# Optimization experiments

Measured on AMD Instinct MI355X. Metric: run time of the kernel, lower is better.

Reference implementation:

```python
import jax, jax.numpy as jnp
import numpy as np

N_ATOMS = 64
N_SAMPLES = 2 ** 15
SAMPLERATE = 22050
N_RES = 4096
N_ROOMS = 8
N_COEFFS = N_SAMPLES // 2 + 1


def make_waves():
    # musical_scale_hz(21, 106, 4096//4) -> 4 waveform families (sine, saw, square, triangle)
    n_steps = N_RES // 4
    midi = np.linspace(21.0, 106.0, n_steps)
    f0 = 440.0 * 2.0 ** ((midi - 69.0) / 12.0)
    rps = ((f0 / (SAMPLERATE / 2.0)) * np.pi).astype(np.float32)
    rad = rps[:, None] * np.arange(N_SAMPLES, dtype=np.float32)[None, :]
    sine = np.sin(rad)
    t = rad / (2.0 * np.pi)
    saw = (2.0 * (t - np.floor(t + 0.5))).astype(np.float32)
    sq = np.sign(sine).astype(np.float32)
    tri = (2.0 * np.abs(saw) - 1.0).astype(np.float32)
    return jnp.asarray(np.concatenate([sine, saw, sq, tri], 0).reshape(1, N_RES, N_SAMPLES))


def pdf2(means, stds, n):
    # gaussian pdf evaluated on linspace(0,1,n); means/stds: (1, A)
    rng = jnp.linspace(0.0, 1.0, n)
    mu = means[..., None]
    sd = stds[..., None]
    return jnp.exp(-0.5 * ((rng - mu) / sd) ** 2) / (sd * jnp.sqrt(2.0 * jnp.pi))


def linear_interp(x, n_out):
    # F.interpolate(mode='linear', align_corners=False) on last axis; x: (b, a, f)
    f = x.shape[-1]
    pos = (jnp.arange(n_out) + 0.5) * (f / n_out) - 0.5
    pos = jnp.clip(pos, 0.0, f - 1)
    i0 = jnp.floor(pos).astype(jnp.int32)
    i1 = jnp.minimum(i0 + 1, f - 1)
    w = (pos - i0).astype(x.dtype)
    return x[..., i0] * (1.0 - w) + x[..., i1] * w


def exponential_decay(decay_values, n_atoms, n_frames, base_resonance, n_samples):
    dv = jax.nn.sigmoid(decay_values.reshape(-1, n_atoms, 1))
    dv = jnp.broadcast_to(dv, (dv.shape[0], n_atoms, n_frames))
    decay = base_resonance + dv * (1.0 - base_resonance) * 0.95
    decay = jnp.exp(jnp.cumsum(jnp.log(decay + 1e-12), axis=-1))
    return linear_interp(decay, n_samples)


def fft_convolve(a, b):
    # zero-pad to 2N, multiply spectra, take first N samples
    n = a.shape[-1]
    pa = jnp.pad(a, ((0, 0), (0, 0), (0, n)))
    pb = jnp.pad(b, ((0, 0), (0, 0), (0, n)))
    spec = jnp.fft.rfft(pa, axis=-1) * jnp.fft.rfft(pb, axis=-1)
    return jnp.fft.irfft(spec, n=2 * n, axis=-1)[..., :n]


def layer_norm(x, w, b, eps=1e-5):
    m = jnp.mean(x, axis=-1, keepdims=True)
    v = jnp.var(x, axis=-1, keepdims=True)
    return (x - m) / jnp.sqrt(v + eps) * w + b


def sparse_softmax_st(x):
    soft = jax.nn.softmax(x, axis=-1)
    hard = jax.nn.one_hot(jnp.argmax(x, axis=-1), x.shape[-1], dtype=x.dtype)
    return hard + soft - jax.lax.stop_gradient(soft)


def model_forward(x, mix, decays, filter_decays, resonance_choice, noise_filter,
                  resonance_filter, resonance_filter2, env, amplitudes, verb_params,
                  noise, waves, ln_w, ln_b, mix_w1, mix_w2, room_w1, room_w2, room_irs):
    overall_mix = jax.nn.softmax(mix, axis=-1)                                   # (1,A,2)
    resonances = jnp.einsum('bar,brn->ban', jax.nn.relu(resonance_choice), waves)  # (1,A,N)

    # band-pass filtered noise (gaussian filter in frequency domain)
    noise_spec = jnp.fft.rfft(noise, axis=-1)
    noise_filt = pdf2(noise_filter[:, :, 0], jnp.abs(noise_filter[:, :, 1]) + 1e-12, N_COEFFS)
    filtered_noise = jnp.fft.irfft(noise_spec * noise_filt, n=N_SAMPLES, axis=-1)

    res_spec = jnp.fft.rfft(resonances, axis=-1)
    rf1 = pdf2(jnp.zeros_like(resonance_filter[:, :, 0]),
               jnp.abs(resonance_filter[:, :, 1]) + 1e-12, N_COEFFS)
    filtered_resonance = jnp.fft.irfft(res_spec * rf1, n=N_SAMPLES, axis=-1)
    rf2 = pdf2(jnp.zeros_like(resonance_filter2[:, :, 0]),
               jnp.abs(resonance_filter2[:, :, 1]) + 1e-12, N_COEFFS)
    filt_res_2 = jnp.fft.irfft(res_spec * rf2, n=N_SAMPLES, axis=-1)

    filt_crossfade = exponential_decay(filter_decays, N_ATOMS, 128, 0.02, N_SAMPLES)
    decay_env = exponential_decay(decays, N_ATOMS, 128, 0.02, N_SAMPLES)
    decaying_resonance = filtered_resonance * decay_env
    decaying_resonance2 = filt_res_2 * decay_env

    # gaussian envelope branch (gaussian_envelope = True)
    envelopes = pdf2(env[:, :, 0], jnp.abs(env[:, :, 1] + 1e-12) * 0.1, N_SAMPLES)
    positioned_noise = filtered_noise * envelopes

    res = fft_convolve(positioned_noise, decaying_resonance)
    res2 = fft_convolve(positioned_noise, decaying_resonance2)
    mixed = filt_crossfade * res + (1.0 - filt_crossfade) * res2

    final = positioned_noise * overall_mix[:, :, 0:1] + mixed * overall_mix[:, :, 1:2]
    final = final / (jnp.linalg.norm(final, axis=-1, keepdims=True) + 1e-8)
    amps = jnp.abs(amplitudes)
    final = final * amps

    # ReverbGenerator: layernorm -> small MLPs -> hard room choice -> fft convolve with IR
    h = layer_norm(verb_params, ln_w, ln_b)
    mix_v = jax.nn.sigmoid(jax.nn.leaky_relu(h @ mix_w1) @ mix_w2)               # (1,A,1)
    room_logits = jax.nn.leaky_relu(h @ room_w1) @ room_w2                        # (1,A,R)
    room = sparse_softmax_st(room_logits)
    ir = jnp.einsum('bar,rn->ban', room, room_irs)
    wet = fft_convolve(final, ir)
    out = final * mix_v + wet * (1.0 - mix_v)
    return out, amps


def setup_inputs() -> dict:
    key = jax.random.key(0)
    ks = jax.random.split(key, 20)
    return {
        'x': jax.random.normal(ks[0], (1, 1), jnp.float32),
        'mix': jax.random.uniform(ks[1], (1, N_ATOMS, 2), jnp.float32),
        'decays': jax.random.uniform(ks[2], (1, N_ATOMS, 1), jnp.float32, -6.0, 6.0),
        'filter_decays': jax.random.uniform(ks[3], (1, N_ATOMS, 1), jnp.float32, -6.0, 6.0),
        'resonance_choice': jax.random.uniform(ks[4], (1, N_ATOMS, N_RES), jnp.float32),
        'noise_filter': jax.random.uniform(ks[5], (1, N_ATOMS, 2), jnp.float32),
        'resonance_filter': jax.random.uniform(ks[6], (1, N_ATOMS, 2), jnp.float32),
        'resonance_filter2': jax.random.uniform(ks[7], (1, N_ATOMS, 2), jnp.float32),
        'env': jax.random.uniform(ks[8], (1, N_ATOMS, 2), jnp.float32),
        'amplitudes': jax.random.uniform(ks[9], (1, N_ATOMS, 1), jnp.float32) ** 2,
        'verb_params': jax.random.uniform(ks[10], (1, N_ATOMS, 4), jnp.float32, -1.0, 1.0),
        'noise': jax.random.uniform(ks[11], (1, N_ATOMS, N_SAMPLES), jnp.float32, -1.0, 1.0),
        'waves': make_waves(),
        'ln_w': jnp.ones((4,), jnp.float32),
        'ln_b': jnp.zeros((4,), jnp.float32),
        'mix_w1': jax.random.normal(ks[12], (4, 4), jnp.float32) * 0.1,
        'mix_w2': jax.random.normal(ks[13], (4, 1), jnp.float32) * 0.1,
        'room_w1': jax.random.normal(ks[14], (4, 4), jnp.float32) * 0.1,
        'room_w2': jax.random.normal(ks[15], (4, N_ROOMS), jnp.float32) * 0.1,
        'room_irs': jax.random.normal(ks[16], (N_ROOMS, N_SAMPLES), jnp.float32) * 0.01,
    }


def reference(x, mix, decays, filter_decays, resonance_choice, noise_filter,
              resonance_filter, resonance_filter2, env, amplitudes, verb_params,
              noise, waves, ln_w, ln_b, mix_w1, mix_w2, room_w1, room_w2, room_irs):
    return model_forward(x, mix, decays, filter_decays, resonance_choice, noise_filter,
                         resonance_filter, resonance_filter2, env, amplitudes, verb_params,
                         noise, waves, ln_w, ln_b, mix_w1, mix_w2, room_w1, room_w2, room_irs)
```

## Files before the change

### kernel.cpp

```cpp
#include <hip/hip_runtime.h>


typedef __attribute__((ext_vector_type(8))) short bf16x8;
typedef __attribute__((ext_vector_type(4))) float f32x4;

constexpr int SC_OM0   = 0;
constexpr int SC_OM1   = 64;
constexpr int SC_NFMU  = 128;
constexpr int SC_NFSD  = 192;
constexpr int SC_RF1SD = 256;
constexpr int SC_RF2SD = 320;
constexpr int SC_ENVMU = 384;
constexpr int SC_ENVSD = 448;
constexpr int SC_AMPS  = 512;
constexpr int SC_MIXV  = 576;
constexpr int SC_ROOM  = 832;
constexpr int SC_PSS   = 1024;
constexpr int SC_DTAB  = 4096;
constexpr int SC_FTAB  = 12288;
constexpr int SC_RPS   = 20480;

constexpr size_t OFF_SCAL = 0;
constexpr size_t OFF_CT   = 65536;
constexpr size_t OFF_P    = 327680;
constexpr size_t OFF_DS   = 8716288;
constexpr size_t OFF_RP   = OFF_DS;
constexpr size_t OFF_W64  = 17104896;
constexpr size_t OFF_NSS  = OFF_W64;
constexpr size_t OFF_W2   = OFF_W64 + 4194304;
constexpr size_t OFF_RSS  = 25493504;
constexpr size_t OFF_FINU = OFF_RSS;
constexpr size_t OFF_W1   = 29687808;
constexpr size_t OFF_FN   = 38076416;
constexpr size_t OFF_FRP  = 40173568;
constexpr size_t OFF_IRS  = 44367872;
constexpr size_t WS_FLOATS= 45416448;

__device__ __forceinline__ float2 cmul(float2 a, float2 b) {
  return make_float2(a.x*b.x - a.y*b.y, a.x*b.y + a.y*b.x);
}

__device__ __forceinline__ short f2bf(float x) {
  unsigned u = __float_as_uint(x);
  u = (u + 0x7FFFu + ((u >> 16) & 1u)) >> 16;
  return (short)u;
}
__device__ __forceinline__ float bf2f(short s) {
  return __uint_as_float((unsigned)(unsigned short)s << 16);
}
__device__ __forceinline__ unsigned pk2(float2 v) {
  return (unsigned)(unsigned short)f2bf(v.x)
       | ((unsigned)(unsigned short)f2bf(v.y) << 16);
}
__device__ __forceinline__ float2 upk2(unsigned u) {
  return make_float2(__uint_as_float(u << 16),
                     __uint_as_float(u & 0xFFFF0000u));
}

__device__ __forceinline__ void dft16(float2 d[16], float ei)
{
  const float CA[4] = {1.0f, 0.92387953251128674f, 0.70710678118654752f, 0.38268343236508977f};
  const float SA[4] = {0.0f, 0.38268343236508977f, 0.70710678118654752f, 0.92387953251128674f};
  const float CB[4] = {1.0f, 0.70710678118654752f, 0.0f, -0.70710678118654752f};
  const float SB[4] = {0.0f, 0.70710678118654752f, 1.0f, 0.70710678118654752f};
  float2 e[16];
  #pragma unroll
  for (int q = 0; q < 4; ++q) {
    float2 x0 = d[q], x1 = d[q+4], x2 = d[q+8], x3 = d[q+12];
    float ca = CA[q], sa = ei*SA[q], cb = CB[q], sb = ei*SB[q];
    float2 sum1 = make_float2(x0.x+x2.x, x0.y+x2.y);
    float2 d1   = make_float2(x0.x-x2.x, x0.y-x2.y);
    float2 dif1 = make_float2(d1.x*ca - d1.y*sa, d1.x*sa + d1.y*ca);
    float2 sum2 = make_float2(x1.x+x3.x, x1.y+x3.y);
    float2 d2   = make_float2(x1.x-x3.x, x1.y-x3.y);
    float2 dt   = make_float2(d2.x*ca - d2.y*sa, d2.x*sa + d2.y*ca);
    float2 dif2 = make_float2(-ei*dt.y, ei*dt.x);
    float2 Dm   = make_float2(sum1.x-sum2.x, sum1.y-sum2.y);
    float2 Dm2  = make_float2(dif1.x-dif2.x, dif1.y-dif2.y);
    e[4*q+0] = make_float2(sum1.x+sum2.x, sum1.y+sum2.y);
    e[4*q+1] = make_float2(dif1.x+dif2.x, dif1.y+dif2.y);
    e[4*q+2] = make_float2(Dm.x*cb - Dm.y*sb, Dm.x*sb + Dm.y*cb);
    e[4*q+3] = make_float2(Dm2.x*cb - Dm2.y*sb, Dm2.x*sb + Dm2.y*cb);
  }
  #pragma unroll
  for (int q = 0; q < 4; ++q) {
    float2 x0 = e[q], x1 = e[q+4], x2 = e[q+8], x3 = e[q+12];
    float2 sum1 = make_float2(x0.x+x2.x, x0.y+x2.y);
    float2 dif1 = make_float2(x0.x-x2.x, x0.y-x2.y);
    float2 sum2 = make_float2(x1.x+x3.x, x1.y+x3.y);
    float2 d2   = make_float2(x1.x-x3.x, x1.y-x3.y);
    float2 dif2 = make_float2(-ei*d2.y, ei*d2.x);
    d[q]    = make_float2(sum1.x+sum2.x, sum1.y+sum2.y);
    d[q+4]  = make_float2(dif1.x+dif2.x, dif1.y+dif2.y);
    d[q+8]  = make_float2(sum1.x-sum2.x, sum1.y-sum2.y);
    d[q+12] = make_float2(dif1.x-dif2.x, dif1.y-dif2.y);
  }
}

__device__ __forceinline__ void twiddleB(float2 d[16], int u, float dir2pi)
{
  float sn1, cs1;
  __sincosf(dir2pi * ((float)u * (1.0f/256.0f)), &sn1, &cs1);
  float2 w1 = make_float2(cs1, sn1);
  float2 tw = w1;
  #pragma unroll
  for (int k = 1; k < 16; ++k) { d[k] = cmul(d[k], tw); tw = cmul(tw, w1); }
}

template<int LEN>
__device__ float2* lds_fft(float2* src, float2* dst,
                           const float2* __restrict__ T256,
                           float dsign, float ei)
{
  constexpr int QB  = LEN >> 2;
  constexpr int FPT = (16 * QB) >> 8;
  constexpr int NST = (LEN == 256) ? 4 : 3;
  int n = LEN, s = 1, ls = 0;
  int sh = (LEN == 256) ? 0 : 1;

  if (LEN == 128) {
    constexpr int HB = LEN >> 1;
    constexpr int BPT = (16 * HB) >> 8;
    __syncthreads();
    #pragma unroll
    for (int b = 0; b < BPT; ++b) {
      int g = threadIdx.x + (b << 8);
      int row = g / HB;
      int beta = g & (HB - 1);
      float2 tj = T256[beta << 1];
      float cs = tj.x, sn = dsign * tj.y;
      float2 av = src[row*LEN + (beta ^ row)];
      float2 bv = src[row*LEN + ((beta + HB) ^ row)];
      float2 sum = make_float2(av.x + bv.x, av.y + bv.y);
      float2 dif = make_float2(av.x - bv.x, av.y - bv.y);
      float2 tw  = make_float2(dif.x*cs - dif.y*sn, dif.x*sn + dif.y*cs);
      dst[row*LEN + ((2*beta)     ^ row)] = sum;
      dst[row*LEN + ((2*beta + 1) ^ row)] = tw;
    }
    float2* t = src; src = dst; dst = t;
    n = 64; s = 2; ls = 1; sh = 2;
  }

  for (int st = 0; st < NST; ++st) {
    __syncthreads();
    #pragma unroll
    for (int b = 0; b < FPT; ++b) {
      int g   = threadIdx.x + (b << 8);
      int row = g / QB;
      int q   = g & (QB - 1);
      int p1  = q >> ls;
      int blo = q & (s - 1);
      int base = row * LEN;
      float2 x0 = src[base + ( q         ^ row)];
      float2 x1 = src[base + ((q +   QB) ^ row)];
      float2 x2 = src[base + ((q + 2*QB) ^ row)];
      float2 x3 = src[base + ((q + 3*QB) ^ row)];
      float2 tA = T256[p1 << sh];
      float caA = tA.x, saA = dsign * tA.y;
      float2 tB = T256[p1 << (sh + 1)];
      float caB = tB.x, saB = dsign * tB.y;
      float2 sum1 = make_float2(x0.x + x2.x, x0.y + x2.y);
      float2 d1   = make_float2(x0.x - x2.x, x0.y - x2.y);
      float2 dif1 = make_float2(d1.x*caA - d1.y*saA, d1.x*saA + d1.y*caA);
      float2 sum2 = make_float2(x1.x + x3.x, x1.y + x3.y);
      float2 d2   = make_float2(x1.x - x3.x, x1.y - x3.y);
      float2 dt   = make_float2(d2.x*caA - d2.y*saA, d2.x*saA + d2.y*caA);
      float2 dif2 = make_float2(-ei * dt.y, ei * dt.x);
      float2 S  = make_float2(sum1.x + sum2.x, sum1.y + sum2.y);
      float2 Dm = make_float2(sum1.x - sum2.x, sum1.y - sum2.y);
      float2 D  = make_float2(Dm.x*caB - Dm.y*saB, Dm.x*saB + Dm.y*caB);
      float2 S2 = make_float2(dif1.x + dif2.x, dif1.y + dif2.y);
      float2 Dm2= make_float2(dif1.x - dif2.x, dif1.y - dif2.y);
      float2 D2 = make_float2(Dm2.x*caB - Dm2.y*saB, Dm2.x*saB + Dm2.y*caB);
      int w0 = (p1 << (ls + 2)) | blo;
      dst[base + ( w0          ^ row)] = S;
      dst[base + ((w0 +     s) ^ row)] = S2;
      dst[base + ((w0 + 2 * s) ^ row)] = D;
      dst[base + ((w0 + 3 * s) ^ row)] = D2;
    }
    float2* t = src; src = dst; dst = t;
    n >>= 2; s <<= 2; ls += 2; sh += 2;
  }
  __syncthreads();
  return src;
}

__global__ __launch_bounds__(256) void k_fft_s256_DsPI(
    unsigned* __restrict__ Ds, unsigned* __restrict__ P,
    unsigned* __restrict__ IRS,
    const unsigned* __restrict__ FRP, const short* __restrict__ fnb,
    const float* __restrict__ rirs, const float* __restrict__ scal)
{
  constexpr int N = 65536, NH = 32768;
  constexpr float FWD = -6.283185307179586f;
  __shared__ float2 X[16*16*17];
  __shared__ float2 T256[256];
  __shared__ float2 TN[256];
  const int mode = (blockIdx.y < 64) ? 0 : ((blockIdx.y < 128) ? 1 : 2);
  const int a = (mode == 0) ? blockIdx.y : ((mode == 1) ? blockIdx.y - 64 : blockIdx.y - 128);
  const int n1base = blockIdx.x << 4;
  const int r = threadIdx.x & 15;
  const int u = threadIdx.x >> 4;

  {
    float ang = FWD * ((float)threadIdx.x * (1.0f/256.0f));
    float sn, cs; __sincosf(ang, &sn, &cs);
    T256[threadIdx.x] = make_float2(cs, sn);
    float ang2 = FWD * ((float)threadIdx.x * (1.0f/(float)N));
    float sn2, cs2; __sincosf(ang2, &sn2, &cs2);
    TN[threadIdx.x] = make_float2(cs2, sn2);
  }

  float emu = 0.f, esd = 1.f, egp = 0.f;
  if (mode == 1) {
    emu = scal[SC_ENVMU + a];
    esd = scal[SC_ENVSD + a];
    egp = 0.3989422804014327f / esd;
  }

  float2 d[16];
  #pragma unroll
  for (int m = 0; m < 16; ++m) {
    int j = u + (m << 4);
    int n = n1base + r + 256 * j;
    float2 v = make_float2(0.0f, 0.0f);
    if (n < NH) {
      if (mode == 0) {
        float pos = ((float)n + 0.5f) * (1.0f/256.0f) - 0.5f;
        pos = fminf(fmaxf(pos, 0.0f), 127.0f);
        int i0 = (int)pos;
        float w = pos - (float)i0;
        int i1 = (i0 + 1 < 127) ? i0 + 1 : 127;
        const float* dt = scal + SC_DTAB + a*128;
        float de = dt[i0]*(1.0f-w) + dt[i1]*w;
        float2 fr = upk2(FRP[(size_t)a * NH + n]);
        v = make_float2(fr.x * de, fr.y * de);
      } else if (mode == 1) {
        float uu = (float)n * (1.0f / 32767.0f);
        float te = (uu - emu) / esd;
        float envv = __expf(-0.5f * te * te) * egp;
        v = make_float2(bf2f(fnb[(size_t)a * NH + n]) * envv, 0.0f);
      } else {
        v = make_float2(rirs[(size_t)a * NH + n], 0.0f);
      }
    }
    d[m] = v;
  }

  dft16(d, -1.0f);
  twiddleB(d, u, FWD);
  #pragma unroll
  for (int k = 0; k < 16; ++k) X[(u*16 + k)*17 + r] = d[k];
  __syncthreads();
  #pragma unroll
  for (int m = 0; m < 16; ++m) d[m] = X[(m*16 + u)*17 + r];
  dft16(d, -1.0f);

  unsigned* outp = (mode == 0) ? Ds : ((mode == 1) ? P : IRS);
  #pragma unroll
  for (int k1 = 0; k1 < 16; ++k1) {
    int j = u + (k1 << 4);
    int n = n1base + r + 256 * j;
    int aa = (n1base + r) * j;
    float2 tw = cmul(T256[(aa >> 8) & 255], TN[aa & 255]);
    outp[(size_t)a * N + n] = pk2(cmul(d[k1], tw));
  }
}

__global__ __launch_bounds__(256) void k_fft_s128_first(
    unsigned* __restrict__ RSs, unsigned* __restrict__ NSs,
    const short* __restrict__ rez, const float* __restrict__ noise)
{
  constexpr int N1 = 128, N = 32768;
  constexpr float FWD = -6.283185307179586f;
  __shared__ float2 X[16*16*17];
  __shared__ float2 T256[256];
  __shared__ float2 TN[128];
  const bool isRS = blockIdx.y < 64;
  const int a = isRS ? blockIdx.y : blockIdx.y - 64;
  const int n1base = blockIdx.x << 4;
  const int r = threadIdx.x & 15;
  const int u = threadIdx.x >> 4;

  {
    float ang = FWD * ((float)threadIdx.x * (1.0f/256.0f));
    float sn, cs; __sincosf(ang, &sn, &cs);
    T256[threadIdx.x] = make_float2(cs, sn);
    if (threadIdx.x < 128) {
      float ang2 = FWD * ((float)threadIdx.x * (1.0f/(float)N));
      float sn2, cs2; __sincosf(ang2, &sn2, &cs2);
      TN[threadIdx.x] = make_float2(cs2, sn2);
    }
  }

  float2 d[16];
  #pragma unroll
  for (int m = 0; m < 16; ++m) {
    int j = u + (m << 4);
    int n = n1base + r + N1 * j;
    float x = isRS ? (bf2f(rez[(size_t)a * N + n]) +
                      bf2f(rez[(size_t)(64 + a) * N + n]))
                   : noise[(size_t)a * N + n];
    d[m] = make_float2(x, 0.0f);
  }

  dft16(d, -1.0f);
  twiddleB(d, u, FWD);
  #pragma unroll
  for (int k = 0; k < 16; ++k) X[(u*16 + k)*17 + r] = d[k];
  __syncthreads();
  #pragma unroll
  for (int m = 0; m < 16; ++m) d[m] = X[(m*16 + u)*17 + r];
  dft16(d, -1.0f);

  unsigned* outp = isRS ? RSs : NSs;
  #pragma unroll
  for (int k1 = 0; k1 < 16; ++k1) {
    int j = u + (k1 << 4);
    int n = n1base + r + N1 * j;
    int aa = (n1base + r) * j;
    float2 tw = cmul(T256[(aa >> 7) & 255], TN[aa & 127]);
    outp[(size_t)a * N + n] = pk2(cmul(d[k1], tw));
  }
}

__global__ __launch_bounds__(256) void k_fft_m128_both(
    const unsigned* __restrict__ RSs, const unsigned* __restrict__ NSs,
    unsigned* __restrict__ W1, unsigned* __restrict__ W2,
    const float* __restrict__ scal)
{
  constexpr int N1 = 128;
  constexpr int N = N1 * 256;
  constexpr int ITERS = (16 * N1) >> 8;
  constexpr int LOG2N1 = 7;
  constexpr float FWD = -6.283185307179586f;
  constexpr float IVD = +6.283185307179586f;
  __shared__ float2 A[16 * N1];
  __shared__ float2 B[16 * N1];
  __shared__ float2 T256[256];
  __shared__ float2 TN[N1];
  const bool isRS = blockIdx.y < 64;
  const int a = isRS ? blockIdx.y : blockIdx.y - 64;
  const int colbase = blockIdx.x << 4;

  {
    float ang = FWD * ((float)threadIdx.x * (1.0f/256.0f));
    float sn, cs; __sincosf(ang, &sn, &cs);
    T256[threadIdx.x] = make_float2(cs, sn);
    if (threadIdx.x < N1) {
      float ang2 = IVD * ((float)threadIdx.x * (1.0f/(float)N));
      float sn2, cs2; __sincosf(ang2, &sn2, &cs2);
      TN[threadIdx.x] = make_float2(cs2, sn2);
    }
  }

  float mu = 0.f, isd1 = 0.f, g1 = 0.f, isd2 = 0.f, g2 = 0.f;
  if (isRS) {
    float s1 = scal[SC_RF1SD + a], s2 = scal[SC_RF2SD + a];
    isd1 = 1.0f/s1; g1 = 0.3989422804014327f/s1;
    isd2 = 1.0f/s2; g2 = 0.3989422804014327f/s2;
  } else {
    float sd = scal[SC_NFSD + a]; mu = scal[SC_NFMU + a];
    isd1 = 1.0f/sd; g1 = 0.3989422804014327f/sd;
  }
  const unsigned* zin = (isRS ? RSs : NSs) + (size_t)a * N;
  unsigned* out = (isRS ? W1 : W2) + (size_t)a * N;

  #pragma unroll
  for (int it = 0; it < ITERS; ++it) {
    int flat = threadIdx.x + (it << 8);
    int c = flat / N1, j = flat & (N1 - 1);
    A[c*N1 + (j ^ c)] = upk2(zin[(size_t)(colbase + c) * N1 + j]);
  }
  float2* cur = lds_fft<N1>(A, B, T256, 1.0f, -1.0f);
  float2* alt = (cur == A) ? B : A;

  #pragma unroll
  for (int it = 0; it < ITERS; ++it) {
    int flat = threadIdx.x + (it << 8);
    int c = flat / N1, j = flat & (N1 - 1);
    int idx = c*N1 + (j ^ c);
    float2 v = cur[idx];
    int k  = (colbase + c) + (j << 8);
    int kk = (k <= N - k) ? k : N - k;
    if (isRS) {
      float fr = (float)kk * (2.0f/(float)N);
      float t1 = fr * isd1, t2 = fr * isd2;
      float ga = __expf(-0.5f * t1 * t1) * g1;
      float gb = __expf(-0.5f * t2 * t2) * g2;
      v = make_float2(v.x*ga - v.y*gb, v.x*gb + v.y*ga);
    } else {
      float t = ((float)kk * (2.0f/(float)N) - mu) * isd1;
      float g = __expf(-0.5f * t * t) * g1;
      v.x *= g; v.y *= g;
    }
    cur[idx] = v;
  }

  float2* r2 = lds_fft<N1>(cur, alt, T256, -1.0f, 1.0f);

  #pragma unroll
  for (int it = 0; it < ITERS; ++it) {
    int flat = threadIdx.x + (it << 8);
    int c = flat / N1, j = flat & (N1 - 1);
    float2 v = r2[c*N1 + (j ^ c)];
    int aa = j * (colbase + c);
    float2 t1 = T256[(aa >> LOG2N1) & 255];
    t1.y = -t1.y;
    float2 tw = cmul(t1, TN[aa & (N1 - 1)]);
    out[(size_t)(colbase + c) * N1 + j] = pk2(cmul(v, tw));
  }
}

__global__ __launch_bounds__(256) void k_fft_s128_last(
    const unsigned* __restrict__ W1, const unsigned* __restrict__ W2,
    unsigned* __restrict__ FRP, short* __restrict__ fnb)
{
  constexpr int N1 = 128, N = 32768;
  constexpr float IVD = +6.283185307179586f;
  constexpr float S32 = 1.0f / 32768.0f;
  __shared__ float2 X[16*16*17];
  const bool isRS = blockIdx.y < 64;
  const int a = isRS ? blockIdx.y : blockIdx.y - 64;
  const int n1base = blockIdx.x << 4;
  const int r = threadIdx.x & 15;
  const int u = threadIdx.x >> 4;

  const unsigned* cb = (isRS ? W1 : W2) + (size_t)a * N;
  float2 d[16];
  #pragma unroll
  for (int m = 0; m < 16; ++m) {
    int j = u + (m << 4);
    d[m] = upk2(cb[n1base + r + N1 * j]);
  }
  dft16(d, 1.0f);
  twiddleB(d, u, IVD);
  #pragma unroll
  for (int k = 0; k < 16; ++k) X[(u*16 + k)*17 + r] = d[k];
  __syncthreads();
  #pragma unroll
  for (int m = 0; m < 16; ++m) d[m] = X[(m*16 + u)*17 + r];
  dft16(d, 1.0f);

  #pragma unroll
  for (int k1 = 0; k1 < 16; ++k1) {
    int j = u + (k1 << 4);
    int n = n1base + r + N1 * j;
    if (isRS) {
      FRP[(size_t)a * N + n] = pk2(make_float2(d[k1].x * S32, d[k1].y * S32));
    } else {
      fnb[(size_t)a * N + n] = f2bf(d[k1].x * S32);
    }
  }
}

__global__ __launch_bounds__(256) void k_fft_mid256dual(
    const unsigned* __restrict__ zin, const unsigned* __restrict__ zin2half,
    unsigned* __restrict__ out1, const int* __restrict__ roomArr)
{
  constexpr int N = 65536;
  constexpr float FWD = -6.283185307179586f;
  constexpr float IVD = +6.283185307179586f;
  __shared__ float2 X[16*16*17];
  __shared__ float2 T256[256];
  __shared__ float2 TN[256];
  const int a = blockIdx.y;
  const int colbase = blockIdx.x << 4;
  const int u  = threadIdx.x & 15;
  const int rc = threadIdx.x >> 4;

  {
    float ang = FWD * ((float)threadIdx.x * (1.0f/256.0f));
    float sn, cs; __sincosf(ang, &sn, &cs);
    T256[threadIdx.x] = make_float2(cs, sn);
    float ang2 = IVD * ((float)threadIdx.x * (1.0f/(float)N));
    float sn2, cs2; __sincosf(ang2, &sn2, &cs2);
    TN[threadIdx.x] = make_float2(cs2, sn2);
  }
  __syncthreads();

  const unsigned* z2 = zin2half + (size_t)(roomArr ? roomArr[a] : a) * N;
  const size_t rowG = (size_t)a * N + (size_t)(colbase + rc) * 256;
  const size_t rowZ2 = (size_t)(colbase + rc) * 256;

  float2 d[16];
  #pragma unroll
  for (int m = 0; m < 16; ++m) d[m] = upk2(zin[rowG + u + (m << 4)]);
  dft16(d, -1.0f);
  twiddleB(d, u, FWD);
  #pragma unroll
  for (int k = 0; k < 16; ++k) X[(rc*16 + k)*17 + u] = d[k];
  #pragma unroll
  for (int m = 0; m < 16; ++m) d[m] = X[(rc*16 + u)*17 + m];
  dft16(d, -1.0f);

  float2 stash[16];
  #pragma unroll
  for (int k = 0; k < 16; ++k) stash[k] = d[k];
  #pragma unroll
  for (int m = 0; m < 16; ++m) d[m] = upk2(z2[rowZ2 + u + (m << 4)]);
  dft16(d, -1.0f);
  twiddleB(d, u, FWD);
  #pragma unroll
  for (int k = 0; k < 16; ++k) X[(rc*16 + k)*17 + u] = d[k];
  #pragma unroll
  for (int m = 0; m < 16; ++m) d[m] = X[(rc*16 + u)*17 + m];
  dft16(d, -1.0f);
  #pragma unroll
  for (int k = 0; k < 16; ++k) d[k] = cmul(stash[k], d[k]);

  dft16(d, 1.0f);
  twiddleB(d, u, IVD);
  #pragma unroll
  for (int k = 0; k < 16; ++k) X[(rc*16 + k)*17 + u] = d[k];
  #pragma unroll
  for (int m = 0; m < 16; ++m) d[m] = X[(rc*16 + u)*17 + m];
  dft16(d, 1.0f);

  #pragma unroll
  for (int k1 = 0; k1 < 16; ++k1) {
    int j = u + (k1 << 4);
    int aa = j * (colbase + rc);
    float2 t1 = T256[(aa >> 8) & 255];
    t1.y = -t1.y;
    float2 tw = cmul(t1, TN[aa & 255]);
    out1[rowG + j] = pk2(cmul(d[k1], tw));
  }
}

__global__ __launch_bounds__(256) void k_fft_out6fwd(
    const unsigned* __restrict__ W64in, const short* __restrict__ fnb,
    float* __restrict__ finU, float* __restrict__ scal,
    unsigned* __restrict__ DsOut)
{
  constexpr int N = 65536, NH = 32768;
  constexpr float FWD = -6.283185307179586f;
  constexpr float IVD = +6.283185307179586f;
  constexpr float S64 = 1.0f / 65536.0f;
  __shared__ float2 X[16*16*17];
  __shared__ float2 T256[256];
  __shared__ float2 TN[256];
  __shared__ float red[256];
  const int a = blockIdx.y;
  const int n1base = blockIdx.x << 4;
  const int r = threadIdx.x & 15;
  const int u = threadIdx.x >> 4;

  {
    float ang = FWD * ((float)threadIdx.x * (1.0f/256.0f));
    float sn, cs; __sincosf(ang, &sn, &cs);
    T256[threadIdx.x] = make_float2(cs, sn);
    float ang2 = FWD * ((float)threadIdx.x * (1.0f/(float)N));
    float sn2, cs2; __sincosf(ang2, &sn2, &cs2);
    TN[threadIdx.x] = make_float2(cs2, sn2);
  }

  const float emu = scal[SC_ENVMU + a];
  const float esd = scal[SC_ENVSD + a];
  const float egp = 0.3989422804014327f / esd;
  const float om0 = scal[SC_OM0 + a], om1 = scal[SC_OM1 + a];
  const float* ft = scal + SC_FTAB + a*128;

  float2 d[16];
  #pragma unroll
  for (int m = 0; m < 16; ++m) {
    int j = u + (m << 4);
    d[m] = upk2(W64in[(size_t)a * N + n1base + r + 256 * j]);
  }
  dft16(d, 1.0f);
  twiddleB(d, u, IVD);
  #pragma unroll
  for (int k = 0; k < 16; ++k) X[(u*16 + k)*17 + r] = d[k];
  __syncthreads();
  #pragma unroll
  for (int m = 0; m < 16; ++m) d[m] = X[(m*16 + u)*17 + r];
  dft16(d, 1.0f);

  float fv[8];
  float ss = 0.0f;
  #pragma unroll
  for (int k1 = 0; k1 < 8; ++k1) {
    int n = n1base + r + 256 * (u + (k1 << 4));
    float resv  = d[k1].x * S64;
    float res2v = d[k1].y * S64;
    float uu = (float)n * (1.0f / 32767.0f);
    float te = (uu - emu) / esd;
    float envv = __expf(-0.5f * te * te) * egp;
    float pnv = bf2f(fnb[(size_t)a * NH + n]) * envv;
    float pos = ((float)n + 0.5f) * (1.0f/256.0f) - 0.5f;
    pos = fminf(fmaxf(pos, 0.0f), 127.0f);
    int i0 = (int)pos;
    float w = pos - (float)i0;
    int i1 = (i0 + 1 < 127) ? i0 + 1 : 127;
    float fc = ft[i0]*(1.0f-w) + ft[i1]*w;
    float f = pnv*om0 + (fc*resv + (1.0f-fc)*res2v)*om1;
    finU[(size_t)a * NH + n] = f;
    fv[k1] = f;
    ss += f * f;
  }
  red[threadIdx.x] = ss;
  __syncthreads();
  for (int s = 128; s > 0; s >>= 1) {
    if (threadIdx.x < s) red[threadIdx.x] += red[threadIdx.x + s];
    __syncthreads();
  }
  if (threadIdx.x == 0) scal[SC_PSS + a*16 + blockIdx.x] = red[0];

  #pragma unroll
  for (int m = 0; m < 16; ++m)
    d[m] = (m < 8) ? make_float2(fv[m], 0.0f) : make_float2(0.0f, 0.0f);
  dft16(d, -1.0f);
  twiddleB(d, u, FWD);
  #pragma unroll
  for (int k = 0; k < 16; ++k) X[(u*16 + k)*17 + r] = d[k];
  __syncthreads();
  #pragma unroll
  for (int m = 0; m < 16; ++m) d[m] = X[(m*16 + u)*17 + r];
  dft16(d, -1.0f);

  #pragma unroll
  for (int k1 = 0; k1 < 16; ++k1) {
    int j = u + (k1 << 4);
    int n = n1base + r + 256 * j;
    int aa = (n1base + r) * j;
    float2 tw = cmul(T256[(aa >> 8) & 255], TN[aa & 255]);
    DsOut[(size_t)a * N + n] = pk2(cmul(d[k1], tw));
  }
}

__global__ __launch_bounds__(256) void k_fft_s256_out3(
    const unsigned* __restrict__ W64in, const float* __restrict__ finU,
    const float* __restrict__ scal, float* __restrict__ out)
{
  constexpr int N = 65536, NH = 32768;
  constexpr float IVD = +6.283185307179586f;
  constexpr float S64 = 1.0f / 65536.0f;
  __shared__ float2 X[16*16*17];
  const int a = blockIdx.y;
  const int n1base = blockIdx.x << 4;
  const int r = threadIdx.x & 15;
  const int u = threadIdx.x >> 4;

  float ss = 0.0f;
  #pragma unroll
  for (int i = 0; i < 16; ++i) ss += scal[SC_PSS + a*16 + i];
  float fscale = scal[SC_AMPS + a] / (sqrtf(ss) + 1e-8f);
  float mixv = scal[SC_MIXV + a];
  float w1 = fscale * (1.0f - mixv);
  float w0 = fscale * mixv;

  float2 d[16];
  #pragma unroll
  for (int m = 0; m < 16; ++m) {
    int j = u + (m << 4);
    d[m] = upk2(W64in[(size_t)a * N + n1base + r + 256 * j]);
  }
  dft16(d, 1.0f);
  twiddleB(d, u, IVD);
  #pragma unroll
  for (int k = 0; k < 16; ++k) X[(u*16 + k)*17 + r] = d[k];
  __syncthreads();
  #pragma unroll
  for (int m = 0; m < 16; ++m) d[m] = X[(m*16 + u)*17 + r];
  dft16(d, 1.0f);

  #pragma unroll
  for (int k1 = 0; k1 < 8; ++k1) {
    int n = n1base + r + 256 * (u + (k1 << 4));
    out[(size_t)a * NH + n] =
        d[k1].x * S64 * w1 + finU[(size_t)a * NH + n] * w0;
  }
}

__global__ void k_packA(const float* __restrict__ rc, short* __restrict__ ctb,
    const float* __restrict__ mix, const float* __restrict__ decays,
    const float* __restrict__ fdec, const float* __restrict__ nf,
    const float* __restrict__ rf1, const float* __restrict__ rf2,
    const float* __restrict__ env, const float* __restrict__ amplitudes,
    const float* __restrict__ verb, const float* __restrict__ ln_w,
    const float* __restrict__ ln_b, const float* __restrict__ mw1,
    const float* __restrict__ mw2, const float* __restrict__ rw1,
    const float* __restrict__ rw2, float* __restrict__ scal,
    float* __restrict__ dout)
{
  int o = blockIdx.x * 256 + threadIdx.x;
  {
    int m = o >> 12, k = o & 4095;
    int s = k >> 2, f = k & 3;
    float v = fmaxf(rc[m*4096 + f*1024 + s], 0.0f);
    ctb[o] = f2bf(v);
  }
  if (blockIdx.x < 4) {
    int idx = blockIdx.x * 256 + threadIdx.x;
    double step = 85.0 / 1023.0;
    double midi = (double)idx * step + 21.0;
    if (idx == 1023) midi = 106.0;
    double f0 = 440.0 * exp2((midi - 69.0) * (1.0 / 12.0));
    scal[SC_RPS + idx] = (float)((f0 / 11025.0) * 3.141592653589793);
  }
  if (blockIdx.x != 0 || threadIdx.x >= 64) return;
  int a = threadIdx.x;
  float m0 = mix[a*2+0], m1 = mix[a*2+1];
  float mx = fmaxf(m0, m1);
  float e0 = expf(m0 - mx), e1 = expf(m1 - mx);
  float inv = 1.0f / (e0 + e1);
  scal[SC_OM0+a] = e0 * inv;
  scal[SC_OM1+a] = e1 * inv;
  scal[SC_NFMU+a] = nf[a*2+0];
  scal[SC_NFSD+a] = fabsf(nf[a*2+1]) + 1e-12f;
  scal[SC_RF1SD+a] = fabsf(rf1[a*2+1]) + 1e-12f;
  scal[SC_RF2SD+a] = fabsf(rf2[a*2+1]) + 1e-12f;
  scal[SC_ENVMU+a] = env[a*2+0];
  scal[SC_ENVSD+a] = fabsf(env[a*2+1] + 1e-12f) * 0.1f;
  float amp = fabsf(amplitudes[a]);
  scal[SC_AMPS+a] = amp;
  dout[2097152 + a] = amp;
  float d  = 0.02f + (1.0f/(1.0f+expf(-decays[a]))) * (0.98f * 0.95f);
  float fd = 0.02f + (1.0f/(1.0f+expf(-fdec[a])))   * (0.98f * 0.95f);
  float pd = 1.0f, pf = 1.0f;
  for (int f = 0; f < 128; ++f) {
    pd *= d; pf *= fd;
    scal[SC_DTAB + a*128 + f] = pd;
    scal[SC_FTAB + a*128 + f] = pf;
  }
  float x0 = verb[a*4+0], x1 = verb[a*4+1], x2 = verb[a*4+2], x3 = verb[a*4+3];
  float mean = (x0+x1+x2+x3) * 0.25f;
  float d0 = x0-mean, d1 = x1-mean, d2 = x2-mean, d3 = x3-mean;
  float var = (d0*d0 + d1*d1 + d2*d2 + d3*d3) * 0.25f;
  float rs = 1.0f / sqrtf(var + 1e-5f);
  float h[4] = { d0*rs*ln_w[0]+ln_b[0], d1*rs*ln_w[1]+ln_b[1],
                 d2*rs*ln_w[2]+ln_b[2], d3*rs*ln_w[3]+ln_b[3] };
  float t[4], u[4];
  for (int j = 0; j < 4; ++j) {
    float s1 = 0.f, s2 = 0.f;
    for (int i2 = 0; i2 < 4; ++i2) {
      s1 += h[i2] * mw1[i2*4 + j];
      s2 += h[i2] * rw1[i2*4 + j];
    }
    t[j] = (s1 > 0.f) ? s1 : 0.01f*s1;
    u[j] = (s2 > 0.f) ? s2 : 0.01f*s2;
  }
  float ml = 0.f;
  for (int j = 0; j < 4; ++j) ml += t[j] * mw2[j];
  scal[SC_MIXV+a] = 1.0f / (1.0f + expf(-ml));
  float best = -1e30f; int bi = 0;
  for (int rr = 0; rr < 8; ++rr) {
    float lg = 0.f;
    for (int j = 0; j < 4; ++j) lg += u[j] * rw2[j*8 + rr];
    if (lg > best) { best = lg; bi = rr; }
  }
  ((int*)scal)[SC_ROOM + a] = bi;
}

__global__ __launch_bounds__(512) void k_gemm_mfma(
    const float* __restrict__ scal, const short* __restrict__ ctb,
    short* __restrict__ rp)
{
  const int t = threadIdx.x;
  const int w = t >> 6, lane = t & 63;
  const int ml = lane & 15, q = lane >> 4;
  const int col = blockIdx.x * 128 + w * 16 + ml;
  const int part = blockIdx.y;

  const float colf = (float)col;
  const float TWO_PI_F = 6.28318530717958647692f;
  const double INV_2PI = 0.15915494309189533577;

  f32x4 acc[4] = {};
  const short* abase = ctb + (size_t)ml * 4096 + (size_t)part * 2048 + q * 8;
  const float* rtab = scal + SC_RPS + part * 512;

  #define WAVE4(rps, b, off) { \
    float rad = (rps) * colf; \
    double dt = (double)rad * INV_2PI; \
    double frd = dt - floor(dt); \
    float sine = __sinf((float)frd * TWO_PI_F); \
    float sq = (rad == 0.0f) ? 0.0f : ((frd < 0.5) ? 1.0f : -1.0f); \
    float tt = rad / TWO_PI_F; \
    float saw = 2.0f * (tt - floorf(tt + 0.5f)); \
    float tri = 2.0f * fabsf(saw) - 1.0f; \
    b[off+0] = f2bf(sine); b[off+1] = f2bf(saw); \
    b[off+2] = f2bf(sq);   b[off+3] = f2bf(tri); }

  for (int kbl = 0; kbl < 64; ++kbl) {
    int sl = kbl * 8 + 2 * q;
    float rps0 = rtab[sl], rps1 = rtab[sl + 1];
    bf16x8 b;
    WAVE4(rps0, b, 0);
    WAVE4(rps1, b, 4);
    const short* ap = abase + (size_t)kbl * 32;
    acc[0] = __builtin_amdgcn_mfma_f32_16x16x32_bf16(*(const bf16x8*)(ap),                   b, acc[0], 0,0,0);
    acc[1] = __builtin_amdgcn_mfma_f32_16x16x32_bf16(*(const bf16x8*)(ap + (size_t)16*4096), b, acc[1], 0,0,0);
    acc[2] = __builtin_amdgcn_mfma_f32_16x16x32_bf16(*(const bf16x8*)(ap + (size_t)32*4096), b, acc[2], 0,0,0);
    acc[3] = __builtin_amdgcn_mfma_f32_16x16x32_bf16(*(const bf16x8*)(ap + (size_t)48*4096), b, acc[3], 0,0,0);
  }
  #undef WAVE4

  #pragma unroll
  for (int mt = 0; mt < 4; ++mt) {
    #pragma unroll
    for (int rr = 0; rr < 4; ++rr) {
      rp[(size_t)(part*64 + mt*16 + q*4 + rr) * 32768 + col] = f2bf(acc[mt][rr]);
    }
  }
}

extern "C" void kernel_launch(void* const* d_in, const int* in_sizes, int n_in,
                              void* d_out, int out_size, void* d_ws, size_t ws_size,
                              hipStream_t stream)
{
  const float* mix   = (const float*)d_in[1];
  const float* dec   = (const float*)d_in[2];
  const float* fdec  = (const float*)d_in[3];
  const float* rc    = (const float*)d_in[4];
  const float* nf    = (const float*)d_in[5];
  const float* rf1   = (const float*)d_in[6];
  const float* rf2   = (const float*)d_in[7];
  const float* env   = (const float*)d_in[8];
  const float* amps  = (const float*)d_in[9];
  const float* verb  = (const float*)d_in[10];
  const float* noise = (const float*)d_in[11];
  const float* lnw   = (const float*)d_in[13];
  const float* lnb   = (const float*)d_in[14];
  const float* mw1   = (const float*)d_in[15];
  const float* mw2   = (const float*)d_in[16];
  const float* rw1   = (const float*)d_in[17];
  const float* rw2   = (const float*)d_in[18];
  const float* rirs  = (const float*)d_in[19];
  float* out = (float*)d_out;
  float* w   = (float*)d_ws;

  if (ws_size < WS_FLOATS * 4ULL) return;

  float*    scal = w + OFF_SCAL;
  short*    ctb  = (short*)(w + OFF_CT);
  short*    rp   = (short*)(w + OFF_RP);
  unsigned* P    = (unsigned*)(w + OFF_P);
  unsigned* Ds   = (unsigned*)(w + OFF_DS);
  unsigned* W64  = (unsigned*)(w + OFF_W64);
  unsigned* RSs  = (unsigned*)(w + OFF_RSS);
  unsigned* NSs  = (unsigned*)(w + OFF_NSS);
  unsigned* W2   = (unsigned*)(w + OFF_W2);
  float*    finU = w + OFF_FINU;
  unsigned* W1   = (unsigned*)(w + OFF_W1);
  short*    fnb  = (short*)(w + OFF_FN);
  unsigned* FRP  = (unsigned*)(w + OFF_FRP);
  unsigned* IRS  = (unsigned*)(w + OFF_IRS);
  const int* room = ((const int*)(w + OFF_SCAL)) + SC_ROOM;

  k_packA<<<1024, 256, 0, stream>>>(rc, ctb, mix, dec, fdec, nf, rf1, rf2, env,
                                    amps, verb, lnw, lnb, mw1, mw2, rw1, rw2,
                                    scal, out);
  k_gemm_mfma<<<dim3(256, 2), 512, 0, stream>>>(scal, ctb, rp);

  k_fft_s128_first<<<dim3(8,128),256,0,stream>>>(RSs, NSs, rp, noise);
  k_fft_m128_both<<<dim3(16,128),256,0,stream>>>(RSs, NSs, W1, W2, scal);
  k_fft_s128_last<<<dim3(8,128),256,0,stream>>>(W1, W2, FRP, fnb);

  k_fft_s256_DsPI<<<dim3(16,136),256,0,stream>>>(Ds, P, IRS, FRP, fnb, rirs, scal);

  k_fft_mid256dual<<<dim3(16,64),256,0,stream>>>(Ds, P, W64, nullptr);

  k_fft_out6fwd<<<dim3(16,64),256,0,stream>>>(W64, fnb, finU, scal, Ds);

  k_fft_mid256dual<<<dim3(16,64),256,0,stream>>>(Ds, IRS, W64, room);

  k_fft_s256_out3<<<dim3(16,64),256,0,stream>>>(W64, finU, scal, out);
}
```

Measured before the change: 268.4 us.

## Replace LDS radix-4 FFT in middle kernel with register 8x16 decomposition

The middle 128-point FFT/filter/IFFT kernel now does each length-128 transform as a register-resident radix-8 pass followed by a radix-16 pass, with one padded LDS transpose between them. This replaces the generic multi-stage LDS ping-pong FFT and its many barriers. The forward 16-point transform, the Gaussian filter and the inverse 16-point transform run back to back in registers. Each block now handles 32 columns instead of 16, halving the grid. The cost is higher register pressure and strided global loads of 8 elements per thread.

```diff
diff --git a/kernel.cpp b/kernel.cpp
--- a/kernel.cpp
+++ b/kernel.cpp
@@ -97,6 +97,49 @@
   }
 }
 
+__device__ __forceinline__ void dft8(float2 d[8], float ei)
+{
+  const float RS = 0.70710678118654752f;
+  float2 E[4], O[4];
+  {
+    float2 s02 = make_float2(d[0].x+d[4].x, d[0].y+d[4].y);
+    float2 m02 = make_float2(d[0].x-d[4].x, d[0].y-d[4].y);
+    float2 s13 = make_float2(d[2].x+d[6].x, d[2].y+d[6].y);
+    float2 m13 = make_float2(d[2].x-d[6].x, d[2].y-d[6].y);
+    float2 im13 = make_float2(-ei*m13.y, ei*m13.x);
+    E[0] = make_float2(s02.x+s13.x, s02.y+s13.y);
+    E[1] = make_float2(m02.x+im13.x, m02.y+im13.y);
+    E[2] = make_float2(s02.x-s13.x, s02.y-s13.y);
+    E[3] = make_float2(m02.x-im13.x, m02.y-im13.y);
+  }
+  {
+    float2 s02 = make_float2(d[1].x+d[5].x, d[1].y+d[5].y);
+    float2 m02 = make_float2(d[1].x-d[5].x, d[1].y-d[5].y);
+    float2 s13 = make_float2(d[3].x+d[7].x, d[3].y+d[7].y);
+    float2 m13 = make_float2(d[3].x-d[7].x, d[3].y-d[7].y);
+    float2 im13 = make_float2(-ei*m13.y, ei*m13.x);
+    O[0] = make_float2(s02.x+s13.x, s02.y+s13.y);
+    O[1] = make_float2(m02.x+im13.x, m02.y+im13.y);
+    O[2] = make_float2(s02.x-s13.x, s02.y-s13.y);
+    O[3] = make_float2(m02.x-im13.x, m02.y-im13.y);
+  }
+  float2 w1 = make_float2(RS, ei*RS);
+  float2 w2 = make_float2(0.0f, ei);
+  float2 w3 = make_float2(-RS, ei*RS);
+  float2 t0 = O[0];
+  float2 t1 = cmul(w1, O[1]);
+  float2 t2 = cmul(w2, O[2]);
+  float2 t3 = cmul(w3, O[3]);
+  d[0] = make_float2(E[0].x+t0.x, E[0].y+t0.y);
+  d[1] = make_float2(E[1].x+t1.x, E[1].y+t1.y);
+  d[2] = make_float2(E[2].x+t2.x, E[2].y+t2.y);
+  d[3] = make_float2(E[3].x+t3.x, E[3].y+t3.y);
+  d[4] = make_float2(E[0].x-t0.x, E[0].y-t0.y);
+  d[5] = make_float2(E[1].x-t1.x, E[1].y-t1.y);
+  d[6] = make_float2(E[2].x-t2.x, E[2].y-t2.y);
+  d[7] = make_float2(E[3].x-t3.x, E[3].y-t3.y);
+}
+
 __device__ __forceinline__ void twiddleB(float2 d[16], int u, float dir2pi)
 {
   float sn1, cs1;
@@ -105,84 +148,6 @@
   float2 tw = w1;
   #pragma unroll
   for (int k = 1; k < 16; ++k) { d[k] = cmul(d[k], tw); tw = cmul(tw, w1); }
-}
-
-template<int LEN>
-__device__ float2* lds_fft(float2* src, float2* dst,
-                           const float2* __restrict__ T256,
-                           float dsign, float ei)
-{
-  constexpr int QB  = LEN >> 2;
-  constexpr int FPT = (16 * QB) >> 8;
-  constexpr int NST = (LEN == 256) ? 4 : 3;
-  int n = LEN, s = 1, ls = 0;
-  int sh = (LEN == 256) ? 0 : 1;
-
-  if (LEN == 128) {
-    constexpr int HB = LEN >> 1;
-    constexpr int BPT = (16 * HB) >> 8;
-    __syncthreads();
-    #pragma unroll
-    for (int b = 0; b < BPT; ++b) {
-      int g = threadIdx.x + (b << 8);
-      int row = g / HB;
-      int beta = g & (HB - 1);
-      float2 tj = T256[beta << 1];
-      float cs = tj.x, sn = dsign * tj.y;
-      float2 av = src[row*LEN + (beta ^ row)];
-      float2 bv = src[row*LEN + ((beta + HB) ^ row)];
-      float2 sum = make_float2(av.x + bv.x, av.y + bv.y);
-      float2 dif = make_float2(av.x - bv.x, av.y - bv.y);
-      float2 tw  = make_float2(dif.x*cs - dif.y*sn, dif.x*sn + dif.y*cs);
-      dst[row*LEN + ((2*beta)     ^ row)] = sum;
-      dst[row*LEN + ((2*beta + 1) ^ row)] = tw;
-    }
-    float2* t = src; src = dst; dst = t;
-    n = 64; s = 2; ls = 1; sh = 2;
-  }
-
-  for (int st = 0; st < NST; ++st) {
-    __syncthreads();
-    #pragma unroll
-    for (int b = 0; b < FPT; ++b) {
-      int g   = threadIdx.x + (b << 8);
-      int row = g / QB;
-      int q   = g & (QB - 1);
-      int p1  = q >> ls;
-      int blo = q & (s - 1);
-      int base = row * LEN;
-      float2 x0 = src[base + ( q         ^ row)];
-      float2 x1 = src[base + ((q +   QB) ^ row)];
-      float2 x2 = src[base + ((q + 2*QB) ^ row)];
-      float2 x3 = src[base + ((q + 3*QB) ^ row)];
-      float2 tA = T256[p1 << sh];
-      float caA = tA.x, saA = dsign * tA.y;
-      float2 tB = T256[p1 << (sh + 1)];
-      float caB = tB.x, saB = dsign * tB.y;
-      float2 sum1 = make_float2(x0.x + x2.x, x0.y + x2.y);
-      float2 d1   = make_float2(x0.x - x2.x, x0.y - x2.y);
-      float2 dif1 = make_float2(d1.x*caA - d1.y*saA, d1.x*saA + d1.y*caA);
-      float2 sum2 = make_float2(x1.x + x3.x, x1.y + x3.y);
-      float2 d2   = make_float2(x1.x - x3.x, x1.y - x3.y);
-      float2 dt   = make_float2(d2.x*caA - d2.y*saA, d2.x*saA + d2.y*caA);
-      float2 dif2 = make_float2(-ei * dt.y, ei * dt.x);
-      float2 S  = make_float2(sum1.x + sum2.x, sum1.y + sum2.y);
-      float2 Dm = make_float2(sum1.x - sum2.x, sum1.y - sum2.y);
-      float2 D  = make_float2(Dm.x*caB - Dm.y*saB, Dm.x*saB + Dm.y*caB);
-      float2 S2 = make_float2(dif1.x + dif2.x, dif1.y + dif2.y);
-      float2 Dm2= make_float2(dif1.x - dif2.x, dif1.y - dif2.y);
-      float2 D2 = make_float2(Dm2.x*caB - Dm2.y*saB, Dm2.x*saB + Dm2.y*caB);
-      int w0 = (p1 << (ls + 2)) | blo;
-      dst[base + ( w0          ^ row)] = S;
-      dst[base + ((w0 +     s) ^ row)] = S2;
-      dst[base + ((w0 + 2 * s) ^ row)] = D;
-      dst[base + ((w0 + 3 * s) ^ row)] = D2;
-    }
-    float2* t = src; src = dst; dst = t;
-    n >>= 2; s <<= 2; ls += 2; sh += 2;
-  }
-  __syncthreads();
-  return src;
 }
 
 __global__ __launch_bounds__(256) void k_fft_s256_DsPI(
@@ -329,28 +294,25 @@
     unsigned* __restrict__ W1, unsigned* __restrict__ W2,
     const float* __restrict__ scal)
 {
-  constexpr int N1 = 128;
-  constexpr int N = N1 * 256;
-  constexpr int ITERS = (16 * N1) >> 8;
-  constexpr int LOG2N1 = 7;
+  constexpr int N = 32768;
   constexpr float FWD = -6.283185307179586f;
   constexpr float IVD = +6.283185307179586f;
-  __shared__ float2 A[16 * N1];
-  __shared__ float2 B[16 * N1];
+  __shared__ float2 L[32*145];
   __shared__ float2 T256[256];
-  __shared__ float2 TN[N1];
+  __shared__ float2 TN[128];
   const bool isRS = blockIdx.y < 64;
   const int a = isRS ? blockIdx.y : blockIdx.y - 64;
-  const int colbase = blockIdx.x << 4;
+  const int colbase = blockIdx.x << 5;
+  const int t = threadIdx.x;
 
   {
-    float ang = FWD * ((float)threadIdx.x * (1.0f/256.0f));
+    float ang = FWD * ((float)t * (1.0f/256.0f));
     float sn, cs; __sincosf(ang, &sn, &cs);
-    T256[threadIdx.x] = make_float2(cs, sn);
-    if (threadIdx.x < N1) {
-      float ang2 = IVD * ((float)threadIdx.x * (1.0f/(float)N));
+    T256[t] = make_float2(cs, sn);
+    if (t < 128) {
+      float ang2 = IVD * ((float)t * (1.0f/(float)N));
       float sn2, cs2; __sincosf(ang2, &sn2, &cs2);
-      TN[threadIdx.x] = make_float2(cs2, sn2);
+      TN[t] = make_float2(cs2, sn2);
     }
   }
 
@@ -364,51 +326,81 @@
     isd1 = 1.0f/sd; g1 = 0.3989422804014327f/sd;
   }
   const unsigned* zin = (isRS ? RSs : NSs) + (size_t)a * N;
-  unsigned* out = (isRS ? W1 : W2) + (size_t)a * N;
-
-  #pragma unroll
-  for (int it = 0; it < ITERS; ++it) {
-    int flat = threadIdx.x + (it << 8);
-    int c = flat / N1, j = flat & (N1 - 1);
-    A[c*N1 + (j ^ c)] = upk2(zin[(size_t)(colbase + c) * N1 + j]);
-  }
-  float2* cur = lds_fft<N1>(A, B, T256, 1.0f, -1.0f);
-  float2* alt = (cur == A) ? B : A;
-
-  #pragma unroll
-  for (int it = 0; it < ITERS; ++it) {
-    int flat = threadIdx.x + (it << 8);
-    int c = flat / N1, j = flat & (N1 - 1);
-    int idx = c*N1 + (j ^ c);
-    float2 v = cur[idx];
-    int k  = (colbase + c) + (j << 8);
-    int kk = (k <= N - k) ? k : N - k;
-    if (isRS) {
-      float fr = (float)kk * (2.0f/(float)N);
-      float t1 = fr * isd1, t2 = fr * isd2;
-      float ga = __expf(-0.5f * t1 * t1) * g1;
-      float gb = __expf(-0.5f * t2 * t2) * g2;
-      v = make_float2(v.x*ga - v.y*gb, v.x*gb + v.y*ga);
-    } else {
-      float t = ((float)kk * (2.0f/(float)N) - mu) * isd1;
-      float g = __expf(-0.5f * t * t) * g1;
-      v.x *= g; v.y *= g;
-    }
-    cur[idx] = v;
-  }
-
-  float2* r2 = lds_fft<N1>(cur, alt, T256, -1.0f, 1.0f);
-
-  #pragma unroll
-  for (int it = 0; it < ITERS; ++it) {
-    int flat = threadIdx.x + (it << 8);
-    int c = flat / N1, j = flat & (N1 - 1);
-    float2 v = r2[c*N1 + (j ^ c)];
-    int aa = j * (colbase + c);
-    float2 t1 = T256[(aa >> LOG2N1) & 255];
-    t1.y = -t1.y;
-    float2 tw = cmul(t1, TN[aa & (N1 - 1)]);
-    out[(size_t)(colbase + c) * N1 + j] = pk2(cmul(v, tw));
+  unsigned* outp = (isRS ? W1 : W2) + (size_t)a * N;
+
+  __syncthreads();
+
+  #pragma unroll
+  for (int pp = 0; pp < 2; ++pp) {
+    int p = t + (pp << 8);
+    int c = p >> 4, n1 = p & 15;
+    float2 d8[8];
+    #pragma unroll
+    for (int n2 = 0; n2 < 8; ++n2)
+      d8[n2] = upk2(zin[(size_t)(colbase + c) * 128 + n1 + (n2 << 4)]);
+    dft8(d8, -1.0f);
+    #pragma unroll
+    for (int k2 = 0; k2 < 8; ++k2) {
+      float2 v = cmul(d8[k2], T256[(k2 * n1) << 1]);
+      L[c*145 + n1*9 + k2] = v;
+    }
+  }
+  __syncthreads();
+
+  {
+    int c = t >> 3, k2 = t & 7;
+    float2 d[16];
+    #pragma unroll
+    for (int n1 = 0; n1 < 16; ++n1) d[n1] = L[c*145 + n1*9 + k2];
+    dft16(d, -1.0f);
+    int col = colbase + c;
+    #pragma unroll
+    for (int k1 = 0; k1 < 16; ++k1) {
+      int j = k2 + (k1 << 3);
+      int k = col + (j << 8);
+      int kk = (k <= N - k) ? k : N - k;
+      float2 v = d[k1];
+      if (isRS) {
+        float fr = (float)kk * (2.0f/(float)N);
+        float t1 = fr * isd1, t2 = fr * isd2;
+        float ga = __expf(-0.5f * t1 * t1) * g1;
+        float gb = __expf(-0.5f * t2 * t2) * g2;
+        v = make_float2(v.x*ga - v.y*gb, v.x*gb + v.y*ga);
+      } else {
+        float tt = ((float)kk * (2.0f/(float)N) - mu) * isd1;
+        float g = __expf(-0.5f * tt * tt) * g1;
+        v.x *= g; v.y *= g;
+      }
+      d[k1] = v;
+    }
+    dft16(d, 1.0f);
+    #pragma unroll
+    for (int n1 = 0; n1 < 16; ++n1) {
+      float2 tw = T256[(k2 * n1) << 1];
+      tw.y = -tw.y;
+      L[c*145 + n1*9 + k2] = cmul(d[n1], tw);
+    }
+  }
+  __syncthreads();
+
+  #pragma unroll
+  for (int pp = 0; pp < 2; ++pp) {
+    int p = t + (pp << 8);
+    int c = p >> 4, n1 = p & 15;
+    float2 d8[8];
+    #pragma unroll
+    for (int k2 = 0; k2 < 8; ++k2) d8[k2] = L[c*145 + n1*9 + k2];
+    dft8(d8, 1.0f);
+    int col = colbase + c;
+    #pragma unroll
+    for (int n2 = 0; n2 < 8; ++n2) {
+      int n = n1 + (n2 << 4);
+      int aa = n * col;
+      float2 t1 = T256[(aa >> 7) & 255];
+      t1.y = -t1.y;
+      float2 tw = cmul(t1, TN[aa & 127]);
+      outp[(size_t)col * 128 + n] = pk2(cmul(d8[n2], tw));
+    }
   }
 }
 
@@ -854,7 +846,7 @@
   k_gemm_mfma<<<dim3(256, 2), 512, 0, stream>>>(scal, ctb, rp);
 
   k_fft_s128_first<<<dim3(8,128),256,0,stream>>>(RSs, NSs, rp, noise);
-  k_fft_m128_both<<<dim3(16,128),256,0,stream>>>(RSs, NSs, W1, W2, scal);
+  k_fft_m128_both<<<dim3(8,128),256,0,stream>>>(RSs, NSs, W1, W2, scal);
   k_fft_s128_last<<<dim3(8,128),256,0,stream>>>(W1, W2, FRP, fnb);
 
   k_fft_s256_DsPI<<<dim3(16,136),256,0,stream>>>(Ds, P, IRS, FRP, fnb, rirs, scal);
```

Measured after the change: 260.8 us. -2.9%, faster.
